# Performance work log

Measured on AMD Instinct MI355X. Metric: run time of the kernel, lower is better.

## Reference

```python
import jax, jax.numpy as jnp
import numpy as np

NEG = -1000000.0  # mask fill value used by the original sequence_mask


def setup_inputs() -> dict:
    key = jax.random.key(0)
    k1, k2, k3, k4 = jax.random.split(key, 4)
    B, Nq, Nk, D = 8, 2048, 2048, 64
    queries = jax.random.normal(k1, (B, Nq, D), dtype=jnp.float32)
    keys = jax.random.normal(k2, (B, Nk, D), dtype=jnp.float32)
    values = jax.random.normal(k3, (B, Nk, D), dtype=jnp.float32)
    valid_lens = jax.random.randint(k4, (B,), 1, Nk + 1, dtype=jnp.int32)
    return {"queries": queries, "keys": keys, "values": values, "valid_lens": valid_lens}


def reference(queries, keys, values, valid_lens):
    d = queries.shape[-1]
    # scores: (B, n_q, n_k)
    scores = jnp.einsum("bqd,bkd->bqk", queries, keys) / jnp.sqrt(jnp.float32(d))
    # mask key positions >= valid_len (per-batch valid length, broadcast over queries)
    nk = scores.shape[-1]
    key_pos = jnp.arange(nk, dtype=jnp.int32)  # (n_k,)
    mask = key_pos[None, None, :] < valid_lens[:, None, None]  # (B, 1->n_q, n_k)
    scores = jnp.where(mask, scores, NEG)
    attn = jax.nn.softmax(scores, axis=-1)
    # dropout is identity in inference mode (no training flag in the original call)
    return jnp.einsum("bqk,bkd->bqd", attn, values)
```

## Files before the change

kernel.cpp:

```cpp
#include <hip/hip_runtime.h>
#include <hip/hip_bf16.h>


typedef __attribute__((ext_vector_type(8))) short bf16x8;
typedef __attribute__((ext_vector_type(8))) unsigned short u16x8;
typedef __attribute__((ext_vector_type(4))) float f32x4;

#define NQ 2048
#define NK 2048
#define DH 64
#define NB 8
#define NSPLIT 16
#define SPLIT_LEN 128
#define L2E 1.44269504088896341f

#define VMCNT(n) asm volatile("s_waitcnt vmcnt(" #n ")" ::: "memory")

__device__ __forceinline__ unsigned short f2bf(float f) {
    union { float f; unsigned int u; } v; v.f = f;
    unsigned int u = v.u;
    u += 0x7FFFu + ((u >> 16) & 1u);
    return (unsigned short)(u >> 16);
}
__device__ __forceinline__ float bf2f(unsigned short u) {
    union { unsigned int u; float f; } v; v.u = ((unsigned int)u) << 16; return v.f;
}
__device__ __forceinline__ unsigned int pack_bf2(float lo, float hi) {
    return ((unsigned int)f2bf(hi) << 16) | (unsigned int)f2bf(lo);
}
__device__ __forceinline__ float fast_exp2(float x) {
#if __has_builtin(__builtin_amdgcn_exp2f)
    return __builtin_amdgcn_exp2f(x);
#else
    return exp2f(x);
#endif
}
__device__ __forceinline__ void gload16(const void* g, void* l) {
    __builtin_amdgcn_global_load_lds(
        (const __attribute__((address_space(1))) void*)g,
        (__attribute__((address_space(3))) void*)l, 16, 0, 0);
}

__global__ __launch_bounds__(256) void prep(const float* __restrict__ K,
                                            const float* __restrict__ Q,
                                            const float* __restrict__ V,
                                            unsigned short* __restrict__ Kbf,
                                            unsigned short* __restrict__ Qbf,
                                            unsigned short* __restrict__ Vt) {
    if (blockIdx.x < 1024) {
        const bool isQ = blockIdx.x >= 512;
        const size_t idx = ((size_t)(blockIdx.x & 511) * 256 + threadIdx.x) * 8;
        const float* src = isQ ? Q : K;
        const float sc = isQ ? 0.125f : 1.0f;
        const float4 a = *reinterpret_cast<const float4*>(src + idx);
        const float4 b = *reinterpret_cast<const float4*>(src + idx + 4);
        bf16x8 o;
        o[0] = (short)f2bf(a.x * sc); o[1] = (short)f2bf(a.y * sc);
        o[2] = (short)f2bf(a.z * sc); o[3] = (short)f2bf(a.w * sc);
        o[4] = (short)f2bf(b.x * sc); o[5] = (short)f2bf(b.y * sc);
        o[6] = (short)f2bf(b.z * sc); o[7] = (short)f2bf(b.w * sc);
        *reinterpret_cast<bf16x8*>((isQ ? Qbf : Kbf) + idx) = o;
    } else {
        __shared__ unsigned short T[64][65];
        const int bid2 = blockIdx.x - 1024;
        const int b  = bid2 >> 5;
        const int k0 = (bid2 & 31) * 64;
        const int t  = threadIdx.x;
        const int r  = t >> 2;
        const int cb = (t & 3) * 16;
        const float* src = V + ((size_t)(b * NK + k0 + r)) * DH + cb;
#pragma unroll
        for (int j4 = 0; j4 < 4; ++j4) {
            const float4 v = *reinterpret_cast<const float4*>(src + j4 * 4);
            T[r][cb + j4 * 4 + 0] = f2bf(v.x);
            T[r][cb + j4 * 4 + 1] = f2bf(v.y);
            T[r][cb + j4 * 4 + 2] = f2bf(v.z);
            T[r][cb + j4 * 4 + 3] = f2bf(v.w);
        }
        __syncthreads();
        unsigned short* dstb = Vt + (size_t)b * DH * NK;
#pragma unroll
        for (int i = 0; i < 2; ++i) {
            const int cc = t + i * 256;
            const int d  = cc >> 3;
            const int kb = (cc & 7) * 8;
            bf16x8 o;
#pragma unroll
            for (int j = 0; j < 8; ++j) o[j] = (short)T[kb + j][d];
            *reinterpret_cast<bf16x8*>(dstb + (size_t)d * NK + k0 + kb) = o;
        }
    }
}

__global__ __launch_bounds__(512, 8) void attn_split(
    const unsigned short* __restrict__ Qbf, const unsigned short* __restrict__ Kbf,
    const unsigned short* __restrict__ Vt, const int* __restrict__ VL,
    float* __restrict__ Lsum, unsigned short* __restrict__ Opart)
{
    __shared__ __align__(16) unsigned char KV[32768];

    const int bid = blockIdx.x;
    const int x   = bid & 7;
    const int k   = bid >> 3;
    const int qg  = k & 15;
    const int cs  = k >> 4;
    const int b   = cs & 7;
    const int s   = ((x - b) & 7) + (cs >> 3) * 8;

    const int vlen  = VL[b];
    const int kv_lo = s * SPLIT_LEN;
    if (kv_lo >= vlen) return;
    const int kv_hi = min(vlen, kv_lo + SPLIT_LEN);
    const int chunk = kv_hi - kv_lo;
    const int ntt   = (chunk + 63) >> 6;

    const int tid  = threadIdx.x;
    const int wv   = tid >> 6;
    const int lane = tid & 63;
    const int g = lane >> 4;
    const int c = lane & 15;
    const int qt = qg * 8 + wv;
    const int swl = (c & 7) << 4;

    const unsigned short* Qb = Qbf + ((size_t)b * NQ + qt * 16) * DH;
    const unsigned char* Kc = (const unsigned char*)(Kbf + ((size_t)b * NK + kv_lo) * DH);
    const unsigned char* Vbase = (const unsigned char*)(Vt + (size_t)b * DH * NK);
    const int vk0b = kv_lo * 2;
    const int a0 = ((2 * (g & 1)) * 16 + c) * 4;
    const int a1 = a0 + 64;

    bf16x8 qf[2];
#pragma unroll
    for (int ks = 0; ks < 2; ++ks)
        qf[ks] = *reinterpret_cast<const bf16x8*>(Qb + (size_t)c * DH + ks * 32 + g * 8);
    __builtin_amdgcn_sched_barrier(0);
    {
        const int p = tid * 16;
        const int a = p ^ (((p >> 7) & 7) << 4);
        const int d = a >> 7, ko = a & 127;
        gload16(Kc + a, KV + p);
        gload16(Vbase + (size_t)d * (NK * 2) + vk0b + ko, KV + 8192 + p);
        __builtin_amdgcn_sched_barrier(0);
        gload16(Kc + 8192 + a, KV + 16384 + p);
        gload16(Vbase + (size_t)d * (NK * 2) + vk0b + 128 + ko, KV + 24576 + p);
        __builtin_amdgcn_sched_barrier(0);
    }

    float l_run = 0.f;

    auto qk_tile = [&](const unsigned char* Kr, int kv0, unsigned int* pk) {
        f32x4 sv[4];
#pragma unroll
        for (int nt4 = 0; nt4 < 4; ++nt4) {
            const int aK = (nt4 * 16 + c) * 128 + g * 16;
            const bf16x8 kf0 = *reinterpret_cast<const bf16x8*>(Kr + (aK ^ swl));
            const bf16x8 kf1 = *reinterpret_cast<const bf16x8*>(Kr + ((aK + 64) ^ swl));
            f32x4 tacc = (f32x4){0.f, 0.f, 0.f, 0.f};
            tacc = __builtin_amdgcn_mfma_f32_16x16x32_bf16(kf0, qf[0], tacc, 0, 0, 0);
            tacc = __builtin_amdgcn_mfma_f32_16x16x32_bf16(kf1, qf[1], tacc, 0, 0, 0);
            sv[nt4] = tacc;
        }
        if (kv0 + 64 > kv_hi) {
#pragma unroll
            for (int nt4 = 0; nt4 < 4; ++nt4)
#pragma unroll
                for (int r = 0; r < 4; ++r)
                    if (kv0 + nt4 * 16 + 4 * g + r >= vlen) sv[nt4][r] = -1e30f;
        }
        float rs = 0.f;
#pragma unroll
        for (int nt4 = 0; nt4 < 4; ++nt4)
#pragma unroll
            for (int r = 0; r < 4; ++r) {
                const float p = fast_exp2(sv[nt4][r] * L2E);
                sv[nt4][r] = p;
                rs += p;
            }
        l_run += rs;
#pragma unroll
        for (int nt4 = 0; nt4 < 4; ++nt4) {
            pk[nt4 * 2]     = pack_bf2(sv[nt4][0], sv[nt4][1]);
            pk[nt4 * 2 + 1] = pack_bf2(sv[nt4][2], sv[nt4][3]);
        }
    };

    auto repack = [&](const unsigned int* pk, bf16x8* pa) {
#pragma unroll
        for (int ks2 = 0; ks2 < 2; ++ks2) {
            union { unsigned int u[4]; bf16x8 v; } out;
#pragma unroll
            for (int w = 0; w < 4; ++w) {
                const int addr = (w >> 1) ? a1 : a0;
                const int lo = __builtin_amdgcn_ds_bpermute(addr, (int)pk[4 * ks2 + (w & 1)]);
                const int hi = __builtin_amdgcn_ds_bpermute(addr, (int)pk[4 * ks2 + 2 + (w & 1)]);
                out.u[w] = (unsigned int)((g >> 1) ? hi : lo);
            }
            pa[ks2] = out.v;
        }
    };

    f32x4 acc[4];
#pragma unroll
    for (int i = 0; i < 4; ++i) acc[i] = (f32x4){0.f, 0.f, 0.f, 0.f};

    auto pv_tile = [&](const unsigned char* Vr, const bf16x8* pa) {
#pragma unroll
        for (int ks2 = 0; ks2 < 2; ++ks2)
#pragma unroll
            for (int ntd = 0; ntd < 4; ++ntd) {
                const int aV = (ntd * 16 + c) * 128 + ks2 * 64 + g * 16;
                const bf16x8 vf = *reinterpret_cast<const bf16x8*>(Vr + (aV ^ swl));
                acc[ntd] = __builtin_amdgcn_mfma_f32_16x16x32_bf16(pa[ks2], vf, acc[ntd], 0, 0, 0);
            }
    };

    VMCNT(3);
    __builtin_amdgcn_s_barrier();
    __builtin_amdgcn_sched_barrier(0);

    unsigned int pkA[8];
    bf16x8 paA[2];
    qk_tile(KV, kv_lo, pkA);
    repack(pkA, paA);

    VMCNT(1);
    __builtin_amdgcn_s_barrier();
    __builtin_amdgcn_sched_barrier(0);

    pv_tile(KV + 8192, paA);
    bf16x8 paB[2];
    if (ntt > 1) {
        unsigned int pkB[8];
        qk_tile(KV + 16384, kv_lo + 64, pkB);
        repack(pkB, paB);
    }

    VMCNT(0);
    __builtin_amdgcn_s_barrier();
    __builtin_amdgcn_sched_barrier(0);

    if (ntt > 1) pv_tile(KV + 24576, paB);

    float lf = l_run;
    lf += __shfl_xor(lf, 16);
    lf += __shfl_xor(lf, 32);

    const size_t pbase = (size_t)(b * NSPLIT + s) * 128 + qt;
    if (lane < 16) Lsum[pbase * 16 + c] = lf;

    u16x8 pk0, pk1;
#pragma unroll
    for (int ntd = 0; ntd < 2; ++ntd)
#pragma unroll
        for (int r = 0; r < 4; ++r) pk0[ntd * 4 + r] = f2bf(acc[ntd][r]);
#pragma unroll
    for (int ntd = 2; ntd < 4; ++ntd)
#pragma unroll
        for (int r = 0; r < 4; ++r) pk1[(ntd - 2) * 4 + r] = f2bf(acc[ntd][r]);
    unsigned short* op = Opart + pbase * 1024 + (size_t)lane * 16;
    *reinterpret_cast<u16x8*>(op)     = pk0;
    *reinterpret_cast<u16x8*>(op + 8) = pk1;
}

__global__ __launch_bounds__(256) void attn_merge(
    const float* __restrict__ Lsum, const unsigned short* __restrict__ Opart,
    const int* __restrict__ VL, float* __restrict__ O)
{
    const int tid  = threadIdx.x;
    const int wv   = tid >> 6;
    const int lane = tid & 63;
    const int g = lane >> 4;
    const int c = lane & 15;
    const int qi = blockIdx.x * 4 + wv;
    const int b  = qi >> 7;
    const int qt = qi & 127;
    const int vlen = VL[b];
    const int nact = min(NSPLIT, (vlen + SPLIT_LEN - 1) / SPLIT_LEN);

    float accv[16];
    float L4[4] = {0.f, 0.f, 0.f, 0.f};
#pragma unroll
    for (int j = 0; j < 16; ++j) accv[j] = 0.f;

    for (int s = 0; s < nact; ++s) {
        const size_t pb = (size_t)(b * NSPLIT + s) * 128 + qt;
        const u16x8* src = reinterpret_cast<const u16x8*>(
            Opart + pb * 1024 + (size_t)lane * 16);
        const u16x8 lo = src[0], hi = src[1];
#pragma unroll
        for (int j = 0; j < 8; ++j) {
            accv[j]     += bf2f(lo[j]);
            accv[8 + j] += bf2f(hi[j]);
        }
        const float* Lp = Lsum + pb * 16 + 4 * g;
#pragma unroll
        for (int r = 0; r < 4; ++r) L4[r] += Lp[r];
    }
    float inv4[4];
#pragma unroll
    for (int r = 0; r < 4; ++r) inv4[r] = 1.0f / L4[r];

    float* Ob = O + ((size_t)(b * NQ + qt * 16)) * DH;
#pragma unroll
    for (int ntd = 0; ntd < 4; ++ntd)
#pragma unroll
        for (int r = 0; r < 4; ++r)
            Ob[(size_t)(4 * g + r) * DH + ntd * 16 + c] = accv[ntd * 4 + r] * inv4[r];
}

__global__ __launch_bounds__(64) void attn_fwd(
    const float* __restrict__ Q, const float* __restrict__ K,
    const float* __restrict__ V, const int* __restrict__ VL,
    float* __restrict__ O)
{
    __shared__ __align__(16) unsigned short Plds[16 * 40];
    const int bid = blockIdx.x;
    const int b  = bid >> 7;
    const int qt = bid & 127;
    const int q0 = qt * 16;
    const int lane = threadIdx.x;
    const int g = lane >> 4;
    const int c = lane & 15;
    const float* Qb = Q + ((size_t)b * NQ + q0) * DH;
    const float* Kb = K + (size_t)b * NK * DH;
    const float* Vb = V + (size_t)b * NK * DH;
    const int vlen = VL[b];
    bf16x8 qf[2];
#pragma unroll
    for (int ks = 0; ks < 2; ++ks) {
        const float* src = Qb + (size_t)c * DH + ks * 32 + g * 8;
#pragma unroll
        for (int e = 0; e < 8; ++e) qf[ks][e] = (short)f2bf(src[e] * 0.125f);
    }
    f32x4 acc[4];
#pragma unroll
    for (int nt = 0; nt < 4; ++nt) acc[nt] = (f32x4){0.f,0.f,0.f,0.f};
    float m_run[4], l_run[4];
#pragma unroll
    for (int r = 0; r < 4; ++r) { m_run[r] = -3.0e38f; l_run[r] = 0.f; }
    const int ntiles = (vlen + 31) / 32;
    for (int kt = 0; kt < ntiles; ++kt) {
        const int kv0 = kt * 32;
        f32x4 s[2] = {{0.f,0.f,0.f,0.f},{0.f,0.f,0.f,0.f}};
#pragma unroll
        for (int nt = 0; nt < 2; ++nt) {
            const float* kp = Kb + (size_t)(kv0 + nt * 16 + c) * DH + g * 8;
#pragma unroll
            for (int ks = 0; ks < 2; ++ks) {
                bf16x8 kf;
#pragma unroll
                for (int e = 0; e < 8; ++e) kf[e] = (short)f2bf(kp[ks * 32 + e]);
                s[nt] = __builtin_amdgcn_mfma_f32_16x16x32_bf16(qf[ks], kf, s[nt], 0, 0, 0);
            }
        }
        const bool msk0 = (kv0 + c)      >= vlen;
        const bool msk1 = (kv0 + 16 + c) >= vlen;
#pragma unroll
        for (int r = 0; r < 4; ++r) {
            if (msk0) s[0][r] = -1e30f;
            if (msk1) s[1][r] = -1e30f;
        }
        float tmax[4];
#pragma unroll
        for (int r = 0; r < 4; ++r) tmax[r] = fmaxf(s[0][r], s[1][r]);
#pragma unroll
        for (int mbit = 1; mbit < 16; mbit <<= 1)
#pragma unroll
            for (int r = 0; r < 4; ++r)
                tmax[r] = fmaxf(tmax[r], __shfl_xor(tmax[r], mbit));
        float p0[4], p1[4];
#pragma unroll
        for (int r = 0; r < 4; ++r) {
            const float mn = fmaxf(m_run[r], tmax[r]);
            const float sc = fast_exp2((m_run[r] - mn) * L2E);
            m_run[r] = mn;
            p0[r] = fast_exp2((s[0][r] - mn) * L2E);
            p1[r] = fast_exp2((s[1][r] - mn) * L2E);
            l_run[r] = l_run[r] * sc + p0[r] + p1[r];
#pragma unroll
            for (int nt = 0; nt < 4; ++nt) acc[nt][r] *= sc;
        }
#pragma unroll
        for (int r = 0; r < 4; ++r) {
            Plds[(4 * g + r) * 40 + c]      = f2bf(p0[r]);
            Plds[(4 * g + r) * 40 + 16 + c] = f2bf(p1[r]);
        }
        asm volatile("s_waitcnt lgkmcnt(0)" ::: "memory");
        const bf16x8 pa = *reinterpret_cast<const bf16x8*>(&Plds[c * 40 + g * 8]);
#pragma unroll
        for (int nt = 0; nt < 4; ++nt) {
            bf16x8 vf;
#pragma unroll
            for (int e = 0; e < 8; ++e)
                vf[e] = (short)f2bf(Vb[(size_t)(kv0 + 8 * g + e) * DH + nt * 16 + c]);
            acc[nt] = __builtin_amdgcn_mfma_f32_16x16x32_bf16(pa, vf, acc[nt], 0, 0, 0);
        }
    }
#pragma unroll
    for (int mbit = 1; mbit < 16; mbit <<= 1)
#pragma unroll
        for (int r = 0; r < 4; ++r)
            l_run[r] += __shfl_xor(l_run[r], mbit);
    float* Ob = O + ((size_t)b * NQ + q0) * DH;
#pragma unroll
    for (int r = 0; r < 4; ++r) {
        const float inv = 1.0f / l_run[r];
#pragma unroll
        for (int nt = 0; nt < 4; ++nt)
            Ob[(size_t)(4 * g + r) * DH + nt * 16 + c] = acc[nt][r] * inv;
    }
}

extern "C" void kernel_launch(void* const* d_in, const int* in_sizes, int n_in,
                              void* d_out, int out_size, void* d_ws, size_t ws_size,
                              hipStream_t stream) {
    const float* Q  = (const float*)d_in[0];
    const float* K  = (const float*)d_in[1];
    const float* V  = (const float*)d_in[2];
    const int*   VL = (const int*)d_in[3];
    float* O = (float*)d_out;

    const size_t KB_OFF = 0;
    const size_t QB_OFF = (size_t)2 << 20;
    const size_t VT_OFF = (size_t)4 << 20;
    const size_t ML_OFF = (size_t)6 << 20;
    const size_t OP_OFF = (size_t)8 << 20;
    const size_t NEED   = OP_OFF + (size_t)NB * NSPLIT * 128 * 1024 * 2;

    if (ws_size >= NEED) {
        char* w = (char*)d_ws;
        unsigned short* Kbf   = (unsigned short*)(w + KB_OFF);
        unsigned short* Qbf   = (unsigned short*)(w + QB_OFF);
        unsigned short* Vtp   = (unsigned short*)(w + VT_OFF);
        float*          Lsum  = (float*)(w + ML_OFF);
        unsigned short* Opart = (unsigned short*)(w + OP_OFF);

        prep<<<1280, 256, 0, stream>>>(K, Q, V, Kbf, Qbf, Vtp);
        attn_split<<<NB * NSPLIT * 16, 512, 0, stream>>>(Qbf, Kbf, Vtp, VL, Lsum, Opart);
        attn_merge<<<256, 256, 0, stream>>>(Lsum, Opart, VL, O);
    } else {
        attn_fwd<<<NB * 128, 64, 0, stream>>>(Q, K, V, VL, O);
    }
}
```

Baseline: 31.88 us.

## Process two KV splits per block to halve split-attention grid and merge work

Each attention block now handles a pair of 128-key splits (s0 and s0+8) in sequence, reusing the same LDS buffer and prefetching the second split's K/V while the first split's last PV tile runs. The grid shrinks from 2048 to 1024 blocks and the partial-output buffer and merge loop are halved. This cuts block launch overhead, Q-fragment reloads and merge traffic. The cost is longer per-block serial work, fewer blocks for latency hiding, and more load imbalance when valid lengths differ.

```diff
diff --git a/kernel.cpp b/kernel.cpp
--- a/kernel.cpp
+++ b/kernel.cpp
@@ -10,7 +10,7 @@
 #define NK 2048
 #define DH 64
 #define NB 8
-#define NSPLIT 16
+#define NPAIR 8
 #define SPLIT_LEN 128
 #define L2E 1.44269504088896341f
 
@@ -103,16 +103,18 @@
     const int x   = bid & 7;
     const int k   = bid >> 3;
     const int qg  = k & 15;
-    const int cs  = k >> 4;
-    const int b   = cs & 7;
-    const int s   = ((x - b) & 7) + (cs >> 3) * 8;
-
-    const int vlen  = VL[b];
-    const int kv_lo = s * SPLIT_LEN;
-    if (kv_lo >= vlen) return;
-    const int kv_hi = min(vlen, kv_lo + SPLIT_LEN);
-    const int chunk = kv_hi - kv_lo;
-    const int ntt   = (chunk + 63) >> 6;
+    const int b   = k >> 4;
+    const int s0  = (x - b) & 7;
+
+    const int vlen = VL[b];
+    const int kv1  = s0 * SPLIT_LEN;
+    if (kv1 >= vlen) return;
+    const int kv_hi1 = min(vlen, kv1 + SPLIT_LEN);
+    const int ntt1   = (kv_hi1 - kv1 + 63) >> 6;
+    const int kv2    = kv1 + 1024;
+    const bool two   = kv2 < vlen;
+    const int kv_hi2 = min(vlen, kv2 + SPLIT_LEN);
+    const int ntt2   = two ? ((kv_hi2 - kv2 + 63) >> 6) : 0;
 
     const int tid  = threadIdx.x;
     const int wv   = tid >> 6;
@@ -123,28 +125,34 @@
     const int swl = (c & 7) << 4;
 
     const unsigned short* Qb = Qbf + ((size_t)b * NQ + qt * 16) * DH;
-    const unsigned char* Kc = (const unsigned char*)(Kbf + ((size_t)b * NK + kv_lo) * DH);
+    const unsigned char* Kc1 = (const unsigned char*)(Kbf + ((size_t)b * NK + kv1) * DH);
+    const unsigned char* Kc2 = Kc1 + 1024 * 128;
     const unsigned char* Vbase = (const unsigned char*)(Vt + (size_t)b * DH * NK);
-    const int vk0b = kv_lo * 2;
+    const int vkb1 = kv1 * 2;
+    const int vkb2 = vkb1 + 2048;
     const int a0 = ((2 * (g & 1)) * 16 + c) * 4;
     const int a1 = a0 + 64;
+
+    const int sp = tid * 16;
+    const int sa = sp ^ (((sp >> 7) & 7) << 4);
+    const int sd = sa >> 7, sko = sa & 127;
+    auto stage3 = [&](const unsigned char* Kc_, int vkb) {
+        gload16(Kc_ + sa, KV + sp);
+        gload16(Vbase + (size_t)sd * (NK * 2) + vkb + sko, KV + 8192 + sp);
+        gload16(Kc_ + 8192 + sa, KV + 16384 + sp);
+    };
+    auto stageVB = [&](int vkb) {
+        gload16(Vbase + (size_t)sd * (NK * 2) + vkb + 128 + sko, KV + 24576 + sp);
+    };
 
     bf16x8 qf[2];
 #pragma unroll
     for (int ks = 0; ks < 2; ++ks)
         qf[ks] = *reinterpret_cast<const bf16x8*>(Qb + (size_t)c * DH + ks * 32 + g * 8);
     __builtin_amdgcn_sched_barrier(0);
-    {
-        const int p = tid * 16;
-        const int a = p ^ (((p >> 7) & 7) << 4);
-        const int d = a >> 7, ko = a & 127;
-        gload16(Kc + a, KV + p);
-        gload16(Vbase + (size_t)d * (NK * 2) + vk0b + ko, KV + 8192 + p);
-        __builtin_amdgcn_sched_barrier(0);
-        gload16(Kc + 8192 + a, KV + 16384 + p);
-        gload16(Vbase + (size_t)d * (NK * 2) + vk0b + 128 + ko, KV + 24576 + p);
-        __builtin_amdgcn_sched_barrier(0);
-    }
+    stage3(Kc1, vkb1);
+    stageVB(vkb1);
+    __builtin_amdgcn_sched_barrier(0);
 
     float l_run = 0.f;
 
@@ -160,7 +168,7 @@
             tacc = __builtin_amdgcn_mfma_f32_16x16x32_bf16(kf1, qf[1], tacc, 0, 0, 0);
             sv[nt4] = tacc;
         }
-        if (kv0 + 64 > kv_hi) {
+        if (kv0 + 64 > vlen) {
 #pragma unroll
             for (int nt4 = 0; nt4 < 4; ++nt4)
 #pragma unroll
@@ -214,38 +222,63 @@
             }
     };
 
+    unsigned int pkA[8];
+    bf16x8 paA[2], paB[2];
+
     VMCNT(3);
     __builtin_amdgcn_s_barrier();
     __builtin_amdgcn_sched_barrier(0);
-
-    unsigned int pkA[8];
-    bf16x8 paA[2];
-    qk_tile(KV, kv_lo, pkA);
+    qk_tile(KV, kv1, pkA);
     repack(pkA, paA);
 
     VMCNT(1);
     __builtin_amdgcn_s_barrier();
     __builtin_amdgcn_sched_barrier(0);
-
     pv_tile(KV + 8192, paA);
-    bf16x8 paB[2];
-    if (ntt > 1) {
+    if (ntt1 > 1) {
         unsigned int pkB[8];
-        qk_tile(KV + 16384, kv_lo + 64, pkB);
+        qk_tile(KV + 16384, kv1 + 64, pkB);
         repack(pkB, paB);
     }
 
     VMCNT(0);
     __builtin_amdgcn_s_barrier();
     __builtin_amdgcn_sched_barrier(0);
-
-    if (ntt > 1) pv_tile(KV + 24576, paB);
+    if (two) stage3(Kc2, vkb2);
+    if (ntt1 > 1) pv_tile(KV + 24576, paB);
+
+    if (two) {
+        __builtin_amdgcn_sched_barrier(0);
+        __builtin_amdgcn_s_barrier();
+        stageVB(vkb2);
+
+        VMCNT(3);
+        __builtin_amdgcn_s_barrier();
+        __builtin_amdgcn_sched_barrier(0);
+        qk_tile(KV, kv2, pkA);
+        repack(pkA, paA);
+
+        VMCNT(1);
+        __builtin_amdgcn_s_barrier();
+        __builtin_amdgcn_sched_barrier(0);
+        pv_tile(KV + 8192, paA);
+        if (ntt2 > 1) {
+            unsigned int pkB[8];
+            qk_tile(KV + 16384, kv2 + 64, pkB);
+            repack(pkB, paB);
+        }
+
+        VMCNT(0);
+        __builtin_amdgcn_s_barrier();
+        __builtin_amdgcn_sched_barrier(0);
+        if (ntt2 > 1) pv_tile(KV + 24576, paB);
+    }
 
     float lf = l_run;
     lf += __shfl_xor(lf, 16);
     lf += __shfl_xor(lf, 32);
 
-    const size_t pbase = (size_t)(b * NSPLIT + s) * 128 + qt;
+    const size_t pbase = (size_t)(b * NPAIR + s0) * 128 + qt;
     if (lane < 16) Lsum[pbase * 16 + c] = lf;
 
     u16x8 pk0, pk1;
@@ -275,7 +308,7 @@
     const int b  = qi >> 7;
     const int qt = qi & 127;
     const int vlen = VL[b];
-    const int nact = min(NSPLIT, (vlen + SPLIT_LEN - 1) / SPLIT_LEN);
+    const int nact = min(NPAIR, (vlen + SPLIT_LEN - 1) / SPLIT_LEN);
 
     float accv[16];
     float L4[4] = {0.f, 0.f, 0.f, 0.f};
@@ -283,7 +316,7 @@
     for (int j = 0; j < 16; ++j) accv[j] = 0.f;
 
     for (int s = 0; s < nact; ++s) {
-        const size_t pb = (size_t)(b * NSPLIT + s) * 128 + qt;
+        const size_t pb = (size_t)(b * NPAIR + s) * 128 + qt;
         const u16x8* src = reinterpret_cast<const u16x8*>(
             Opart + pb * 1024 + (size_t)lane * 16);
         const u16x8 lo = src[0], hi = src[1];
@@ -425,7 +458,7 @@
     const size_t VT_OFF = (size_t)4 << 20;
     const size_t ML_OFF = (size_t)6 << 20;
     const size_t OP_OFF = (size_t)8 << 20;
-    const size_t NEED   = OP_OFF + (size_t)NB * NSPLIT * 128 * 1024 * 2;
+    const size_t NEED   = OP_OFF + (size_t)NB * NPAIR * 128 * 1024 * 2;
 
     if (ws_size >= NEED) {
         char* w = (char*)d_ws;
@@ -436,7 +469,7 @@
         unsigned short* Opart = (unsigned short*)(w + OP_OFF);
 
         prep<<<1280, 256, 0, stream>>>(K, Q, V, Kbf, Qbf, Vtp);
-        attn_split<<<NB * NSPLIT * 16, 512, 0, stream>>>(Qbf, Kbf, Vtp, VL, Lsum, Opart);
+        attn_split<<<NB * NPAIR * 16, 512, 0, stream>>>(Qbf, Kbf, Vtp, VL, Lsum, Opart);
         attn_merge<<<256, 256, 0, stream>>>(Lsum, Opart, VL, O);
     } else {
         attn_fwd<<<NB * 128, 64, 0, stream>>>(Q, K, V, VL, O);
```

Result: slower. 33.43 us (+4.9%).
